# Kernel tuning notes

Hardware: AMD Instinct MI355X
Metric: run time of the kernel (lower is better)

Reference implementation:

```python
import jax, jax.numpy as jnp
import numpy as np

B, N, C, L = 32, 1024, 1024, 16  # batch, pixels (HW), channels, visual tokens


def setup_inputs() -> dict:
    key = jax.random.key(0)
    ks = jax.random.split(key, 18)
    s = lambda fan_in: 1.0 / np.sqrt(fan_in)
    def lin(kw, kb, fin, fout):
        W = jax.random.uniform(kw, (fin, fout), jnp.float32, -s(fin), s(fin))
        b = jax.random.uniform(kb, (fout,), jnp.float32, -s(fin), s(fin))
        return W, b
    tok_W, tok_b = lin(ks[0], ks[1], C, L)          # tokenizer pointwise conv
    key_W, key_b = lin(ks[2], ks[3], C, C // 2)     # transformer key proj
    query_W, query_b = lin(ks[4], ks[5], C, C // 2) # transformer query proj
    f1_W, f1_b = lin(ks[6], ks[7], C, C)            # FFN 1
    f2_W, f2_b = lin(ks[8], ks[9], C, C)            # FFN 2
    q_W, q_b = lin(ks[10], ks[11], C, C)            # projector W_q
    k_W, k_b = lin(ks[12], ks[13], C, C)            # projector W_k
    feature_map = jax.random.normal(ks[14], (B, N, C), jnp.float32)
    T_in = jnp.zeros((B, L, C), jnp.float32)  # unused by FilterBasedTokenizer
    return dict(feature_map=feature_map, T_in=T_in,
                tok_W=tok_W, tok_b=tok_b, key_W=key_W, key_b=key_b,
                query_W=query_W, query_b=query_b, f1_W=f1_W, f1_b=f1_b,
                f2_W=f2_W, f2_b=f2_b, q_W=q_W, q_b=q_b, k_W=k_W, k_b=k_b)


def reference(feature_map, T_in, tok_W, tok_b, key_W, key_b, query_W, query_b,
              f1_W, f1_b, f2_W, f2_b, q_W, q_b, k_W, k_b):
    X = feature_map  # [B, N, C]
    # --- FilterBasedTokenizer: softmax over pixel dim, aggregate pixels -> tokens
    proj = X @ tok_W + tok_b                         # [B, N, L]
    attn = jax.nn.softmax(proj, axis=1)              # softmax over N (dim=1)
    T = jnp.einsum('bnl,bnc->blc', attn, X)          # [B, L, C]
    # --- Transformer block on visual tokens
    k = T @ key_W + key_b                            # [B, L, C/2]
    q = T @ query_W + query_b                        # [B, L, C/2]
    scores = jnp.einsum('bld,bmd->blm', k, q)        # [B, L, L]
    T_dash = T + jax.nn.softmax(scores, axis=2) @ T  # self-attn residual
    T_out = T_dash + (jax.nn.relu(T_dash @ f1_W + f1_b) @ f2_W + f2_b)
    # --- Projector: pixels attend to tokens
    sim = jnp.einsum('bnc,blc->bnl', X @ q_W + q_b, T_out @ k_W + k_b)  # [B, N, L]
    X_out = X + jax.nn.softmax(sim, axis=2) @ T_out  # [B, N, C]
    return (X_out, T_out)
```

## Files before the change

kernel.cpp:

```cpp
#include <hip/hip_runtime.h>
#include <hip/hip_bf16.h>
#include <stdint.h>

#define BB 32
#define NN 1024
#define CC 1024
#define LL 16

typedef __attribute__((ext_vector_type(4))) float f32x4;
typedef __attribute__((ext_vector_type(8))) short short8;
typedef __attribute__((ext_vector_type(4))) unsigned short ushort4v;

__device__ __forceinline__ unsigned short f2bf(float f) {
  union { float f; unsigned u; } v; v.f = f;
  unsigned r = v.u + 0x7FFF + ((v.u >> 16) & 1);
  return (unsigned short)(r >> 16);
}
__device__ __forceinline__ float bf2f(unsigned short h) {
  union { unsigned u; float f; } v; v.u = ((unsigned)h) << 16; return v.f;
}

__global__ __launch_bounds__(256) void wprep(
    const float* __restrict__ keyW, const float* __restrict__ queryW,
    const float* __restrict__ f1W, const float* __restrict__ f2W,
    const float* __restrict__ kW, const float* __restrict__ qW,
    const float* __restrict__ tokW, const float* __restrict__ keyb,
    const float* __restrict__ queryb,
    unsigned short* __restrict__ WkqT, unsigned short* __restrict__ f1WT,
    unsigned short* __restrict__ f2WT, unsigned short* __restrict__ kWT,
    unsigned short* __restrict__ qWbf, unsigned short* __restrict__ tokWT,
    float* __restrict__ biaskq)
{
  int z = blockIdx.z;
  int tx = threadIdx.x, ty = threadIdx.y;
  if (z == 5) {
    int gid = (blockIdx.y * 32 + blockIdx.x) * 256 + ty * 32 + tx;
    if (gid < 16384) {
      int l = gid >> 10, c = gid & 1023;
      tokWT[gid] = f2bf(tokW[c * 16 + l]);
    } else if (gid < 17408) {
      int i = gid - 16384;
      biaskq[i] = (i < 512) ? keyb[i] : queryb[i - 512];
    }
    return;
  }
  if (z == 4) {
#pragma unroll
    for (int i = 0; i < 4; ++i) {
      int row = blockIdx.y * 32 + ty + 8 * i;
      int col = blockIdx.x * 32 + tx;
      qWbf[row * 1024 + col] = f2bf(qW[row * 1024 + col]);
    }
    return;
  }
  __shared__ float tile[32][33];
  int j0 = blockIdx.x * 32, k0 = blockIdx.y * 32;
  const float* src = (z == 1) ? f1W : (z == 2) ? f2W : kW;
#pragma unroll
  for (int i = 0; i < 4; ++i) {
    int k = k0 + ty + 8 * i;
    int j = j0 + tx;
    float v;
    if (z == 0) v = (j < 512) ? keyW[k * 512 + j] : queryW[k * 512 + (j - 512)];
    else        v = src[k * 1024 + j];
    tile[ty + 8 * i][tx] = v;
  }
  __syncthreads();
  unsigned short* dst = (z == 0) ? WkqT : (z == 1) ? f1WT : (z == 2) ? f2WT : kWT;
#pragma unroll
  for (int i = 0; i < 4; ++i) {
    int j = j0 + ty + 8 * i;
    dst[j * 1024 + k0 + tx] = f2bf(tile[tx][ty + 8 * i]);
  }
}

__global__ __launch_bounds__(256) void proj_mfma(
    const float* __restrict__ X, const unsigned short* __restrict__ Wt,
    const float* __restrict__ bias, float* __restrict__ out)
{
  __shared__ __align__(16) char sp[16384];
  int tid = threadIdx.x, wid = tid >> 6, lane = tid & 63;
  int lr = lane & 15, hi = lane >> 4;
  int pix0 = blockIdx.x * 64;
  int b = pix0 >> 10;
  int row = tid >> 2, seg = tid & 3;
  const float* xr = X + (size_t)(pix0 + row) * 1024 + seg * 32;
  const unsigned short* Wb = Wt + (size_t)lr * 1024 + hi * 8;
  int wbyte[4];
#pragma unroll
  for (int u = 0; u < 4; ++u)
    wbyte[u] = row * 256 + (((seg * 64 + u * 16) ^ ((row & 7) << 4)));
  int arow = wid * 16 + lr;
  int rbyte = arow * 256;
  int rx = (arow & 7) << 4;
  f32x4 acc = (f32x4)0.f;
  for (int k0 = 0; k0 < 1024; k0 += 128) {
    f32x4 v[8];
#pragma unroll
    for (int i = 0; i < 8; ++i) v[i] = *(const f32x4*)(xr + k0 + i * 4);
    __syncthreads();
#pragma unroll
    for (int u = 0; u < 4; ++u) {
      short8 pk;
      pk[0] = (short)f2bf(v[2*u][0]);   pk[1] = (short)f2bf(v[2*u][1]);
      pk[2] = (short)f2bf(v[2*u][2]);   pk[3] = (short)f2bf(v[2*u][3]);
      pk[4] = (short)f2bf(v[2*u+1][0]); pk[5] = (short)f2bf(v[2*u+1][1]);
      pk[6] = (short)f2bf(v[2*u+1][2]); pk[7] = (short)f2bf(v[2*u+1][3]);
      *(short8*)(sp + wbyte[u]) = pk;
    }
    __syncthreads();
#pragma unroll
    for (int kk = 0; kk < 4; ++kk) {
      short8 af = *(const short8*)(sp + rbyte + (((kk * 64 + hi * 16) ^ rx)));
      short8 bf = *(const short8*)(Wb + k0 + kk * 32);
      acc = __builtin_amdgcn_mfma_f32_16x16x32_bf16(af, bf, acc, 0, 0, 0);
    }
  }
  int pixb = pix0 + wid * 16 + hi * 4;
  float bv = bias[lr];
#pragma unroll
  for (int rr = 0; rr < 4; ++rr) {
    int pix = pixb + rr;
    out[((size_t)b * 16 + lr) * 1024 + (pix & 1023)] = acc[rr] + bv;
  }
}

__global__ __launch_bounds__(256) void softmax_n(float* __restrict__ projT) {
  float* row = projT + (size_t)blockIdx.x * NN;
  int t = threadIdx.x;
  f32x4 v = ((f32x4*)row)[t];
  float m = fmaxf(fmaxf(v[0], v[1]), fmaxf(v[2], v[3]));
#pragma unroll
  for (int msk = 32; msk >= 1; msk >>= 1) m = fmaxf(m, __shfl_xor(m, msk));
  __shared__ float redm[4], reds[4];
  if ((t & 63) == 0) redm[t >> 6] = m;
  __syncthreads();
  m = fmaxf(fmaxf(redm[0], redm[1]), fmaxf(redm[2], redm[3]));
  f32x4 e;
  e[0] = __expf(v[0] - m); e[1] = __expf(v[1] - m);
  e[2] = __expf(v[2] - m); e[3] = __expf(v[3] - m);
  float s = e[0] + e[1] + e[2] + e[3];
#pragma unroll
  for (int msk = 32; msk >= 1; msk >>= 1) s += __shfl_xor(s, msk);
  if ((t & 63) == 0) reds[t >> 6] = s;
  __syncthreads();
  s = reds[0] + reds[1] + reds[2] + reds[3];
  float inv = 1.f / s;
  e[0] *= inv; e[1] *= inv; e[2] *= inv; e[3] *= inv;
  ((f32x4*)row)[t] = e;
}

__global__ __launch_bounds__(256) void tpart_kernel(
    const float* __restrict__ X, const float* __restrict__ attnT,
    unsigned short* __restrict__ TpartBf)
{
  int b = blockIdx.y, ch = blockIdx.x;
  int n0 = ch * 128;
  __shared__ float att[128][16];
  int tid = threadIdx.x;
#pragma unroll
  for (int i = 0; i < 2; ++i) {
    int fi = tid + 256 * i;
    int l = fi >> 5, n4 = (fi & 31) << 2;
    f32x4 a = *(const f32x4*)&attnT[((size_t)b * 16 + l) * 1024 + n0 + n4];
    att[n4 + 0][l] = a[0]; att[n4 + 1][l] = a[1];
    att[n4 + 2][l] = a[2]; att[n4 + 3][l] = a[3];
  }
  __syncthreads();
  f32x4 acc[16];
#pragma unroll
  for (int l = 0; l < 16; ++l) acc[l] = (f32x4)0.f;
  const float* xp = X + ((size_t)b * 1024 + n0) * 1024 + tid * 4;
#pragma unroll 4
  for (int n = 0; n < 128; ++n) {
    f32x4 xv = *(const f32x4*)(xp + (size_t)n * 1024);
    const f32x4* ar = (const f32x4*)&att[n][0];
    f32x4 a0 = ar[0], a1 = ar[1], a2 = ar[2], a3 = ar[3];
    acc[0]  += a0[0]*xv; acc[1]  += a0[1]*xv; acc[2]  += a0[2]*xv; acc[3]  += a0[3]*xv;
    acc[4]  += a1[0]*xv; acc[5]  += a1[1]*xv; acc[6]  += a1[2]*xv; acc[7]  += a1[3]*xv;
    acc[8]  += a2[0]*xv; acc[9]  += a2[1]*xv; acc[10] += a2[2]*xv; acc[11] += a2[3]*xv;
    acc[12] += a3[0]*xv; acc[13] += a3[1]*xv; acc[14] += a3[2]*xv; acc[15] += a3[3]*xv;
  }
  unsigned short* op = TpartBf + (size_t)(b * 8 + ch) * 16 * 1024 + tid * 4;
#pragma unroll
  for (int l = 0; l < 16; ++l) {
    f32x4 s = acc[l];
    ushort4v h; h[0]=f2bf(s[0]); h[1]=f2bf(s[1]); h[2]=f2bf(s[2]); h[3]=f2bf(s[3]);
    *(ushort4v*)(op + (size_t)l * 1024) = h;
  }
}

__global__ void treduce(const unsigned short* __restrict__ TpartBf,
                        float* __restrict__ T, unsigned short* __restrict__ Tbf) {
  int f = blockIdx.x * 256 + threadIdx.x;
  int b = f >> 12, w = f & 4095;
  f32x4 s = (f32x4)0.f;
#pragma unroll
  for (int ch = 0; ch < 8; ++ch) {
    ushort4v h = ((const ushort4v*)TpartBf)[(size_t)(b * 8 + ch) * 4096 + w];
    s[0] += bf2f(h[0]); s[1] += bf2f(h[1]); s[2] += bf2f(h[2]); s[3] += bf2f(h[3]);
  }
  ((f32x4*)T)[f] = s;
  ushort4v h; h[0]=f2bf(s[0]); h[1]=f2bf(s[1]); h[2]=f2bf(s[2]); h[3]=f2bf(s[3]);
  ((ushort4v*)Tbf)[f] = h;
}

template<int RELU, int HAS_BIAS, int HAS_RES, int STORE_F32, int STORE_BF16>
__global__ __launch_bounds__(256) void gemm32x64(
    const unsigned short* __restrict__ A, const unsigned short* __restrict__ Bm,
    const float* __restrict__ bias, const float* __restrict__ res,
    float* __restrict__ outF, unsigned short* __restrict__ outB)
{
  const int K = 1024;
  __shared__ __align__(16) char sh[12288];
  char* Asp = sh;
  char* Bsp = sh + 4096;
  int tid = threadIdx.x, wid = tid >> 6, lane = tid & 63;
  int lr = lane & 15, hi = lane >> 4;
  int m0 = blockIdx.x * 32, n0 = blockIdx.y * 64;
  int arow = tid >> 3, acol = (tid & 7) * 8;
  int brow = tid >> 2, bcol = (tid & 3) * 16;
  const unsigned short* Ap = A + (size_t)(m0 + arow) * K + acol;
  const unsigned short* Bp = Bm + (size_t)(n0 + brow) * K + bcol;
  int aw  = arow * 128 + (((acol * 2) ^ ((arow & 7) << 4)));
  int bw0 = brow * 128 + (((bcol * 2) ^ ((brow & 7) << 4)));
  int bw1 = brow * 128 + ((((bcol * 2) + 16) ^ ((brow & 7) << 4)));
  short8 aR[2]; short8 bR[2][2];
  aR[0]    = *(const short8*)(Ap);
  bR[0][0] = *(const short8*)(Bp);
  bR[0][1] = *(const short8*)(Bp + 8);
  aR[1]    = *(const short8*)(Ap + 64);
  bR[1][0] = *(const short8*)(Bp + 64);
  bR[1][1] = *(const short8*)(Bp + 72);
  f32x4 acc[2];
  acc[0] = (f32x4)0.f; acc[1] = (f32x4)0.f;
  int wm = (wid >> 1) * 16, wn = (wid & 1) * 32;
  int arb = (wm + lr) * 128, arx = ((wm + lr) & 7) << 4;
  for (int s = 0; s < 16; ++s) {
    __syncthreads();
    *(short8*)(Asp + aw)  = aR[s & 1];
    *(short8*)(Bsp + bw0) = bR[s & 1][0];
    *(short8*)(Bsp + bw1) = bR[s & 1][1];
    __syncthreads();
    if (s + 2 < 16) {
      int k0 = (s + 2) * 64;
      aR[s & 1]    = *(const short8*)(Ap + k0);
      bR[s & 1][0] = *(const short8*)(Bp + k0);
      bR[s & 1][1] = *(const short8*)(Bp + k0 + 8);
    }
#pragma unroll
    for (int kk = 0; kk < 2; ++kk) {
      short8 af = *(const short8*)(Asp + arb + (((kk * 64 + hi * 16) ^ arx)));
#pragma unroll
      for (int sn = 0; sn < 2; ++sn) {
        int br = wn + sn * 16 + lr;
        short8 bf = *(const short8*)(Bsp + br * 128 + (((kk * 64 + hi * 16) ^ ((br & 7) << 4))));
        acc[sn] = __builtin_amdgcn_mfma_f32_16x16x32_bf16(af, bf, acc[sn], 0, 0, 0);
      }
    }
  }
  int row0 = m0 + wm + hi * 4;
#pragma unroll
  for (int sn = 0; sn < 2; ++sn) {
    int col = n0 + wn + sn * 16 + lr;
    float bv_ = HAS_BIAS ? bias[col] : 0.f;
#pragma unroll
    for (int rr = 0; rr < 4; ++rr) {
      float x = acc[sn][rr] + bv_;
      if (RELU) x = fmaxf(x, 0.f);
      size_t idx = (size_t)(row0 + rr) * 1024 + col;
      if (HAS_RES) x += res[idx];
      if (STORE_F32) outF[idx] = x;
      if (STORE_BF16) outB[idx] = f2bf(x);
    }
  }
}

__global__ __launch_bounds__(256) void scores_tdash(
    const float* __restrict__ kq, const float* __restrict__ T,
    float* __restrict__ Tdash, unsigned short* __restrict__ Tdbf)
{
  int cs = blockIdx.x, b = blockIdx.y;
  int c0 = cs * 128;
  __shared__ float Ts[16][128];
  int tid = threadIdx.x, lane = tid & 63;
#pragma unroll
  for (int i = 0; i < 2; ++i) {
    int fi = tid + 256 * i;
    int rrow = fi >> 5, c4 = (fi & 31) * 4;
    *(f32x4*)&Ts[rrow][c4] = *(const f32x4*)&T[((size_t)b * 16 + rrow) * 1024 + c0 + c4];
  }
  __syncthreads();
  int l = tid >> 4, m = tid & 15;
  const float* krow = kq + ((size_t)b * 16 + l) * 1024;
  const float* qrow = kq + ((size_t)b * 16 + m) * 1024 + 512;
  float s = 0.f;
#pragma unroll 8
  for (int d = 0; d < 512; d += 4) {
    f32x4 kv = *(const f32x4*)(krow + d);
    f32x4 qv = *(const f32x4*)(qrow + d);
    s += kv[0]*qv[0] + kv[1]*qv[1] + kv[2]*qv[2] + kv[3]*qv[3];
  }
  float mx = s;
  mx = fmaxf(mx, __shfl_xor(mx, 1)); mx = fmaxf(mx, __shfl_xor(mx, 2));
  mx = fmaxf(mx, __shfl_xor(mx, 4)); mx = fmaxf(mx, __shfl_xor(mx, 8));
  float e = __expf(s - mx);
  float sum = e;
  sum += __shfl_xor(sum, 1); sum += __shfl_xor(sum, 2);
  sum += __shfl_xor(sum, 4); sum += __shfl_xor(sum, 8);
  float pv = e / sum;
  float pl[16];
#pragma unroll
  for (int i = 0; i < 16; ++i) pl[i] = __shfl(pv, (lane & 48) + i);
  float* od = Tdash + ((size_t)b * 16 + l) * 1024 + c0;
  unsigned short* ob = Tdbf + ((size_t)b * 16 + l) * 1024 + c0;
#pragma unroll
  for (int h = 0; h < 2; ++h) {
    int c = m * 8 + h * 4;
    f32x4 o = *(const f32x4*)&Ts[l][c];
#pragma unroll
    for (int mm = 0; mm < 16; ++mm) {
      f32x4 tv = *(const f32x4*)&Ts[mm][c];
      o += pl[mm] * tv;
    }
    *(f32x4*)(od + c) = o;
    ushort4v hh; hh[0]=f2bf(o[0]); hh[1]=f2bf(o[1]); hh[2]=f2bf(o[2]); hh[3]=f2bf(o[3]);
    *(ushort4v*)(ob + c) = hh;
  }
}

__global__ __launch_bounds__(256) void r_kernel(
    const unsigned short* __restrict__ Tkbf, const float* __restrict__ qb,
    float* __restrict__ r)
{
  int row = blockIdx.x * 4 + (threadIdx.x >> 6);
  int lane = threadIdx.x & 63;
  const unsigned short* p = Tkbf + (size_t)row * CC;
  float s = 0.f;
#pragma unroll
  for (int h = 0; h < 2; ++h) {
    int d0 = lane * 8 + h * 512;
    short8 v = *(const short8*)&p[d0];
#pragma unroll
    for (int jj = 0; jj < 8; ++jj)
      s += bf2f((unsigned short)v[jj]) * qb[d0 + jj];
  }
#pragma unroll
  for (int msk = 32; msk >= 1; msk >>= 1) s += __shfl_xor(s, msk);
  if (lane == 0) r[row] = s;
}

__global__ __launch_bounds__(256) void sim_out_kernel(
    const float* __restrict__ X, const unsigned short* __restrict__ Gt,
    const float* __restrict__ rbias, const float* __restrict__ Tout,
    float* __restrict__ Xout)
{
  __shared__ __align__(16) char sp[16384];
  __shared__ float Ps[64][16];
  int tid = threadIdx.x, wid = tid >> 6, lane = tid & 63;
  int lr = lane & 15, hi = lane >> 4;
  int pix0 = blockIdx.x * 64 + blockIdx.y * 1024;
  int b = blockIdx.y;
  int row = tid >> 2, seg = tid & 3;
  const float* xr = X + (size_t)(pix0 + row) * 1024 + seg * 32;
  const unsigned short* Wb = Gt + (size_t)b * 16 * 1024 + (size_t)lr * 1024 + hi * 8;
  int wbyte[4];
#pragma unroll
  for (int u = 0; u < 4; ++u)
    wbyte[u] = row * 256 + (((seg * 64 + u * 16) ^ ((row & 7) << 4)));
  int arow = wid * 16 + lr;
  int rbyte = arow * 256;
  int rx = (arow & 7) << 4;
  f32x4 acc = (f32x4)0.f;
  for (int k0 = 0; k0 < 1024; k0 += 128) {
    f32x4 v[8];
#pragma unroll
    for (int i = 0; i < 8; ++i) v[i] = *(const f32x4*)(xr + k0 + i * 4);
    __syncthreads();
#pragma unroll
    for (int u = 0; u < 4; ++u) {
      short8 pk;
      pk[0] = (short)f2bf(v[2*u][0]);   pk[1] = (short)f2bf(v[2*u][1]);
      pk[2] = (short)f2bf(v[2*u][2]);   pk[3] = (short)f2bf(v[2*u][3]);
      pk[4] = (short)f2bf(v[2*u+1][0]); pk[5] = (short)f2bf(v[2*u+1][1]);
      pk[6] = (short)f2bf(v[2*u+1][2]); pk[7] = (short)f2bf(v[2*u+1][3]);
      *(short8*)(sp + wbyte[u]) = pk;
    }
    __syncthreads();
#pragma unroll
    for (int kk = 0; kk < 4; ++kk) {
      short8 af = *(const short8*)(sp + rbyte + (((kk * 64 + hi * 16) ^ rx)));
      short8 bf = *(const short8*)(Wb + k0 + kk * 32);
      acc = __builtin_amdgcn_mfma_f32_16x16x32_bf16(af, bf, acc, 0, 0, 0);
    }
  }
  float bv = rbias[b * 16 + lr];
  int prow = wid * 16 + hi * 4;
#pragma unroll
  for (int rr = 0; rr < 4; ++rr) {
    float vv = acc[rr] + bv;
    float mx = vv;
    mx = fmaxf(mx, __shfl_xor(mx, 1)); mx = fmaxf(mx, __shfl_xor(mx, 2));
    mx = fmaxf(mx, __shfl_xor(mx, 4)); mx = fmaxf(mx, __shfl_xor(mx, 8));
    float e = __expf(vv - mx);
    float ss = e;
    ss += __shfl_xor(ss, 1); ss += __shfl_xor(ss, 2);
    ss += __shfl_xor(ss, 4); ss += __shfl_xor(ss, 8);
    Ps[prow + rr][lr] = e / ss;
  }
  __syncthreads();
  int c4 = tid * 4;
  f32x4 tsr[16];
#pragma unroll
  for (int l = 0; l < 16; ++l)
    tsr[l] = *(const f32x4*)&Tout[((size_t)b * 16 + l) * 1024 + c4];
  const float* xp = X + (size_t)pix0 * 1024 + c4;
  float* op = Xout + (size_t)pix0 * 1024 + c4;
#pragma unroll 2
  for (int n = 0; n < 64; ++n) {
    f32x4 xv = *(const f32x4*)(xp + (size_t)n * 1024);
    const f32x4* pr = (const f32x4*)&Ps[n][0];
    f32x4 p0 = pr[0], p1 = pr[1], p2 = pr[2], p3 = pr[3];
    f32x4 o = xv;
    o += p0[0]*tsr[0];  o += p0[1]*tsr[1];  o += p0[2]*tsr[2];  o += p0[3]*tsr[3];
    o += p1[0]*tsr[4];  o += p1[1]*tsr[5];  o += p1[2]*tsr[6];  o += p1[3]*tsr[7];
    o += p2[0]*tsr[8];  o += p2[1]*tsr[9];  o += p2[2]*tsr[10]; o += p2[3]*tsr[11];
    o += p3[0]*tsr[12]; o += p3[1]*tsr[13]; o += p3[2]*tsr[14]; o += p3[3]*tsr[15];
    *(f32x4*)(op + (size_t)n * 1024) = o;
  }
}

extern "C" void kernel_launch(void* const* d_in, const int* in_sizes, int n_in,
                              void* d_out, int out_size, void* d_ws, size_t ws_size,
                              hipStream_t stream)
{
  const float* X      = (const float*)d_in[0];
  const float* tokW   = (const float*)d_in[2];
  const float* tokB   = (const float*)d_in[3];
  const float* keyW   = (const float*)d_in[4];
  const float* keyB   = (const float*)d_in[5];
  const float* queryW = (const float*)d_in[6];
  const float* queryB = (const float*)d_in[7];
  const float* f1W    = (const float*)d_in[8];
  const float* f1B    = (const float*)d_in[9];
  const float* f2W    = (const float*)d_in[10];
  const float* f2B    = (const float*)d_in[11];
  const float* qW     = (const float*)d_in[12];
  const float* qB     = (const float*)d_in[13];
  const float* kW     = (const float*)d_in[14];
  const float* kB     = (const float*)d_in[15];

  float* Xout = (float*)d_out;
  float* Tout = (float*)d_out + (size_t)BB * NN * CC;

  char* ws = (char*)d_ws;
  size_t off = 0;
  auto alloc_f = [&](size_t n) { float* pp = (float*)(ws + off); off += n * 4; return pp; };
  float* attn   = alloc_f(524288);
  float* Tbuf   = alloc_f(524288);
  float* kqbuf  = alloc_f(524288);
  float* Tdash  = alloc_f(524288);
  float* rbuf   = alloc_f(1024);
  float* biaskq = alloc_f(1024);
  auto alloc_h = [&](size_t n) { unsigned short* pp = (unsigned short*)(ws + off); off += n * 2; return pp; };
  unsigned short* TpartBf = alloc_h(4194304);
  unsigned short* Tbf    = alloc_h(524288);
  unsigned short* Tdbf   = alloc_h(524288);
  unsigned short* Hbf    = alloc_h(524288);
  unsigned short* Toutbf = alloc_h(524288);
  unsigned short* Tkbf   = alloc_h(524288);
  unsigned short* Gtbf   = alloc_h(524288);
  unsigned short* WkqT   = alloc_h(1048576);
  unsigned short* f1WT   = alloc_h(1048576);
  unsigned short* f2WT   = alloc_h(1048576);
  unsigned short* kWT    = alloc_h(1048576);
  unsigned short* qWbf   = alloc_h(1048576);
  unsigned short* tokWT  = alloc_h(16384);
  (void)ws_size; (void)in_sizes; (void)n_in; (void)out_size;

  wprep<<<dim3(32, 32, 6), dim3(32, 8), 0, stream>>>(keyW, queryW, f1W, f2W, kW, qW,
                                                     tokW, keyB, queryB,
                                                     WkqT, f1WT, f2WT, kWT, qWbf, tokWT, biaskq);
  proj_mfma<<<dim3(512), 256, 0, stream>>>(X, tokWT, tokB, attn);
  softmax_n<<<512, 256, 0, stream>>>(attn);
  tpart_kernel<<<dim3(8, 32), 256, 0, stream>>>(X, attn, TpartBf);
  treduce<<<512, 256, 0, stream>>>(TpartBf, Tbuf, Tbf);
  gemm32x64<0,1,0,1,0><<<dim3(16, 16), 256, 0, stream>>>(Tbf, WkqT, biaskq, nullptr, kqbuf, nullptr);
  scores_tdash<<<dim3(8, 32), 256, 0, stream>>>(kqbuf, Tbuf, Tdash, Tdbf);
  gemm32x64<1,1,0,0,1><<<dim3(16, 16), 256, 0, stream>>>(Tdbf, f1WT, f1B, nullptr, nullptr, Hbf);
  gemm32x64<0,1,1,1,1><<<dim3(16, 16), 256, 0, stream>>>(Hbf, f2WT, f2B, Tdash, Tout, Toutbf);
  gemm32x64<0,1,0,0,1><<<dim3(16, 16), 256, 0, stream>>>(Toutbf, kWT, kB, nullptr, nullptr, Tkbf);
  r_kernel<<<128, 256, 0, stream>>>(Tkbf, qB, rbuf);
  gemm32x64<0,0,0,0,1><<<dim3(16, 16), 256, 0, stream>>>(Tkbf, qWbf, nullptr, nullptr, nullptr, Gtbf);
  sim_out_kernel<<<dim3(16, 32), 256, 0, stream>>>(X, Gtbf, rbuf, Tout, Xout);
}
```

Measured before the change: 210.6 us.

## Fuse tokenizer with online softmax and run chain as one cooperative kernel

The projection, softmax over pixels and token aggregation are merged into one kernel that emits per-chunk unnormalized partial tokens plus local max and sum statistics, which are combined flash-style in a merge stage. The remaining small GEMMs, scores, r and sim_out stages run inside a single cooperative kernel of 256 blocks separated by grid syncs, replacing about ten separate launches. This removes the attention buffer round trip and most per-launch gaps. In exchange, sim_out now uses only 256 blocks with 128 pixels each, which lowers parallelism for the largest memory-bound stage, and the code depends on cooperative launch support.

```diff
diff --git a/kernel.cpp b/kernel.cpp
--- a/kernel.cpp
+++ b/kernel.cpp
@@ -1,6 +1,9 @@
 #include <hip/hip_runtime.h>
 #include <hip/hip_bf16.h>
+#include <hip/hip_cooperative_groups.h>
 #include <stdint.h>
+
+namespace cg = cooperative_groups;
 
 #define BB 32
 #define NN 1024
@@ -74,33 +77,38 @@
   }
 }
 
-__global__ __launch_bounds__(256) void proj_mfma(
-    const float* __restrict__ X, const unsigned short* __restrict__ Wt,
-    const float* __restrict__ bias, float* __restrict__ out)
+__global__ __launch_bounds__(256) void tok_fused(
+    const float* __restrict__ X, const unsigned short* __restrict__ tokWT,
+    const float* __restrict__ tokB, unsigned short* __restrict__ Tp,
+    float* __restrict__ Mloc, float* __restrict__ Sloc)
 {
-  __shared__ __align__(16) char sp[16384];
+  __shared__ __align__(16) char sp[32768];
+  __shared__ float E[128][16];
+  __shared__ float redm[4][16];
+  __shared__ float reds[4][16];
   int tid = threadIdx.x, wid = tid >> 6, lane = tid & 63;
   int lr = lane & 15, hi = lane >> 4;
-  int pix0 = blockIdx.x * 64;
-  int b = pix0 >> 10;
-  int row = tid >> 2, seg = tid & 3;
-  const float* xr = X + (size_t)(pix0 + row) * 1024 + seg * 32;
-  const unsigned short* Wb = Wt + (size_t)lr * 1024 + hi * 8;
-  int wbyte[4];
-#pragma unroll
-  for (int u = 0; u < 4; ++u)
-    wbyte[u] = row * 256 + (((seg * 64 + u * 16) ^ ((row & 7) << 4)));
-  int arow = wid * 16 + lr;
-  int rbyte = arow * 256;
-  int rx = (arow & 7) << 4;
-  f32x4 acc = (f32x4)0.f;
+  int b = blockIdx.y, ch = blockIdx.x;
+  int pix0 = b * 1024 + ch * 128;
+  int row = tid >> 1, half = tid & 1;
+  const float* xr = X + (size_t)(pix0 + row) * 1024 + half * 64;
+  const unsigned short* Wb = tokWT + lr * 1024 + hi * 8;
+  int wbyte[8];
+#pragma unroll
+  for (int u = 0; u < 8; ++u)
+    wbyte[u] = row * 256 + (((half * 128 + u * 16) ^ ((row & 7) << 4)));
+  int arow0 = wid * 32;
+  int ar0 = arow0 + lr, ar1 = arow0 + 16 + lr;
+  int arb0 = ar0 * 256, arx0 = (ar0 & 7) << 4;
+  int arb1 = ar1 * 256, arx1 = (ar1 & 7) << 4;
+  f32x4 acc0 = (f32x4)0.f, acc1 = (f32x4)0.f;
   for (int k0 = 0; k0 < 1024; k0 += 128) {
-    f32x4 v[8];
-#pragma unroll
-    for (int i = 0; i < 8; ++i) v[i] = *(const f32x4*)(xr + k0 + i * 4);
+    f32x4 v[16];
+#pragma unroll
+    for (int i = 0; i < 16; ++i) v[i] = *(const f32x4*)(xr + k0 + i * 4);
     __syncthreads();
 #pragma unroll
-    for (int u = 0; u < 4; ++u) {
+    for (int u = 0; u < 8; ++u) {
       short8 pk;
       pk[0] = (short)f2bf(v[2*u][0]);   pk[1] = (short)f2bf(v[2*u][1]);
       pk[2] = (short)f2bf(v[2*u][2]);   pk[3] = (short)f2bf(v[2*u][3]);
@@ -111,113 +119,126 @@
     __syncthreads();
 #pragma unroll
     for (int kk = 0; kk < 4; ++kk) {
-      short8 af = *(const short8*)(sp + rbyte + (((kk * 64 + hi * 16) ^ rx)));
-      short8 bf = *(const short8*)(Wb + k0 + kk * 32);
-      acc = __builtin_amdgcn_mfma_f32_16x16x32_bf16(af, bf, acc, 0, 0, 0);
-    }
-  }
-  int pixb = pix0 + wid * 16 + hi * 4;
-  float bv = bias[lr];
+      short8 bfv = *(const short8*)(Wb + k0 + kk * 32);
+      short8 a0 = *(const short8*)(sp + arb0 + (((kk * 64 + hi * 16) ^ arx0)));
+      short8 a1 = *(const short8*)(sp + arb1 + (((kk * 64 + hi * 16) ^ arx1)));
+      acc0 = __builtin_amdgcn_mfma_f32_16x16x32_bf16(a0, bfv, acc0, 0, 0, 0);
+      acc1 = __builtin_amdgcn_mfma_f32_16x16x32_bf16(a1, bfv, acc1, 0, 0, 0);
+    }
+  }
+  float tb = tokB[lr];
+  float sv[8];
+#pragma unroll
+  for (int rr = 0; rr < 4; ++rr) { sv[rr] = acc0[rr] + tb; sv[4 + rr] = acc1[rr] + tb; }
+  float pm = sv[0];
+#pragma unroll
+  for (int i = 1; i < 8; ++i) pm = fmaxf(pm, sv[i]);
+  pm = fmaxf(pm, __shfl_xor(pm, 16));
+  pm = fmaxf(pm, __shfl_xor(pm, 32));
+  if (hi == 0) redm[wid][lr] = pm;
+  __syncthreads();
+  float m = fmaxf(fmaxf(redm[0][lr], redm[1][lr]), fmaxf(redm[2][lr], redm[3][lr]));
+  float ev[8]; float ps = 0.f;
+#pragma unroll
+  for (int i = 0; i < 8; ++i) { ev[i] = __expf(sv[i] - m); ps += ev[i]; }
+  ps += __shfl_xor(ps, 16); ps += __shfl_xor(ps, 32);
+  if (hi == 0) reds[wid][lr] = ps;
 #pragma unroll
   for (int rr = 0; rr < 4; ++rr) {
-    int pix = pixb + rr;
-    out[((size_t)b * 16 + lr) * 1024 + (pix & 1023)] = acc[rr] + bv;
-  }
-}
-
-__global__ __launch_bounds__(256) void softmax_n(float* __restrict__ projT) {
-  float* row = projT + (size_t)blockIdx.x * NN;
-  int t = threadIdx.x;
-  f32x4 v = ((f32x4*)row)[t];
-  float m = fmaxf(fmaxf(v[0], v[1]), fmaxf(v[2], v[3]));
-#pragma unroll
-  for (int msk = 32; msk >= 1; msk >>= 1) m = fmaxf(m, __shfl_xor(m, msk));
-  __shared__ float redm[4], reds[4];
-  if ((t & 63) == 0) redm[t >> 6] = m;
+    E[arow0 + hi * 4 + rr][lr] = ev[rr];
+    E[arow0 + 16 + hi * 4 + rr][lr] = ev[4 + rr];
+  }
   __syncthreads();
-  m = fmaxf(fmaxf(redm[0], redm[1]), fmaxf(redm[2], redm[3]));
-  f32x4 e;
-  e[0] = __expf(v[0] - m); e[1] = __expf(v[1] - m);
-  e[2] = __expf(v[2] - m); e[3] = __expf(v[3] - m);
-  float s = e[0] + e[1] + e[2] + e[3];
-#pragma unroll
-  for (int msk = 32; msk >= 1; msk >>= 1) s += __shfl_xor(s, msk);
-  if ((t & 63) == 0) reds[t >> 6] = s;
-  __syncthreads();
-  s = reds[0] + reds[1] + reds[2] + reds[3];
-  float inv = 1.f / s;
-  e[0] *= inv; e[1] *= inv; e[2] *= inv; e[3] *= inv;
-  ((f32x4*)row)[t] = e;
-}
-
-__global__ __launch_bounds__(256) void tpart_kernel(
-    const float* __restrict__ X, const float* __restrict__ attnT,
-    unsigned short* __restrict__ TpartBf)
-{
-  int b = blockIdx.y, ch = blockIdx.x;
-  int n0 = ch * 128;
-  __shared__ float att[128][16];
-  int tid = threadIdx.x;
-#pragma unroll
-  for (int i = 0; i < 2; ++i) {
-    int fi = tid + 256 * i;
-    int l = fi >> 5, n4 = (fi & 31) << 2;
-    f32x4 a = *(const f32x4*)&attnT[((size_t)b * 16 + l) * 1024 + n0 + n4];
-    att[n4 + 0][l] = a[0]; att[n4 + 1][l] = a[1];
-    att[n4 + 2][l] = a[2]; att[n4 + 3][l] = a[3];
-  }
-  __syncthreads();
-  f32x4 acc[16];
-#pragma unroll
-  for (int l = 0; l < 16; ++l) acc[l] = (f32x4)0.f;
-  const float* xp = X + ((size_t)b * 1024 + n0) * 1024 + tid * 4;
+  if (tid < 16) {
+    float sl = reds[0][tid] + reds[1][tid] + reds[2][tid] + reds[3][tid];
+    Mloc[(b * 8 + ch) * 16 + tid] = m;
+    Sloc[(b * 8 + ch) * 16 + tid] = sl;
+  }
+  f32x4 a16[16];
+#pragma unroll
+  for (int l = 0; l < 16; ++l) a16[l] = (f32x4)0.f;
+  const float* xp = X + (size_t)pix0 * 1024 + tid * 4;
 #pragma unroll 4
   for (int n = 0; n < 128; ++n) {
     f32x4 xv = *(const f32x4*)(xp + (size_t)n * 1024);
-    const f32x4* ar = (const f32x4*)&att[n][0];
+    const f32x4* ar = (const f32x4*)&E[n][0];
     f32x4 a0 = ar[0], a1 = ar[1], a2 = ar[2], a3 = ar[3];
-    acc[0]  += a0[0]*xv; acc[1]  += a0[1]*xv; acc[2]  += a0[2]*xv; acc[3]  += a0[3]*xv;
-    acc[4]  += a1[0]*xv; acc[5]  += a1[1]*xv; acc[6]  += a1[2]*xv; acc[7]  += a1[3]*xv;
-    acc[8]  += a2[0]*xv; acc[9]  += a2[1]*xv; acc[10] += a2[2]*xv; acc[11] += a2[3]*xv;
-    acc[12] += a3[0]*xv; acc[13] += a3[1]*xv; acc[14] += a3[2]*xv; acc[15] += a3[3]*xv;
-  }
-  unsigned short* op = TpartBf + (size_t)(b * 8 + ch) * 16 * 1024 + tid * 4;
+    a16[0]  += a0[0]*xv; a16[1]  += a0[1]*xv; a16[2]  += a0[2]*xv; a16[3]  += a0[3]*xv;
+    a16[4]  += a1[0]*xv; a16[5]  += a1[1]*xv; a16[6]  += a1[2]*xv; a16[7]  += a1[3]*xv;
+    a16[8]  += a2[0]*xv; a16[9]  += a2[1]*xv; a16[10] += a2[2]*xv; a16[11] += a2[3]*xv;
+    a16[12] += a3[0]*xv; a16[13] += a3[1]*xv; a16[14] += a3[2]*xv; a16[15] += a3[3]*xv;
+  }
+  unsigned short* op = Tp + ((size_t)(b * 8 + ch) * 16) * 1024 + tid * 4;
 #pragma unroll
   for (int l = 0; l < 16; ++l) {
-    f32x4 s = acc[l];
+    f32x4 s = a16[l];
     ushort4v h; h[0]=f2bf(s[0]); h[1]=f2bf(s[1]); h[2]=f2bf(s[2]); h[3]=f2bf(s[3]);
     *(ushort4v*)(op + (size_t)l * 1024) = h;
   }
 }
 
-__global__ void treduce(const unsigned short* __restrict__ TpartBf,
-                        float* __restrict__ T, unsigned short* __restrict__ Tbf) {
-  int f = blockIdx.x * 256 + threadIdx.x;
-  int b = f >> 12, w = f & 4095;
-  f32x4 s = (f32x4)0.f;
+struct ChainArgs {
+  const unsigned short* Tp; const float* Mloc; const float* Sloc;
+  float* Tbuf; unsigned short* Tbf;
+  const unsigned short* WkqT; const float* biaskq; float* kqbuf;
+  float* Tdash; unsigned short* Tdbf;
+  const unsigned short* f1WT; const float* f1B; unsigned short* Hbf;
+  const unsigned short* f2WT; const float* f2B; float* Tout; unsigned short* Toutbf;
+  const unsigned short* kWT; const float* kB; unsigned short* Tkbf;
+  const unsigned short* qWbf; const float* qB; float* rbuf;
+  unsigned short* Gtbf;
+  const float* X; float* Xout;
+};
+
+__device__ __forceinline__ void tmerge_stage(int bid, const ChainArgs& a) {
+  int tid = threadIdx.x;
+  int g = bid * 2 + (tid >> 7);
+  int b = g >> 4, l = g & 15;
+  int j = tid & 127;
+  float M = -1e30f;
+#pragma unroll
+  for (int ch = 0; ch < 8; ++ch) M = fmaxf(M, a.Mloc[(b * 8 + ch) * 16 + l]);
+  float w[8]; float denom = 0.f;
 #pragma unroll
   for (int ch = 0; ch < 8; ++ch) {
-    ushort4v h = ((const ushort4v*)TpartBf)[(size_t)(b * 8 + ch) * 4096 + w];
-    s[0] += bf2f(h[0]); s[1] += bf2f(h[1]); s[2] += bf2f(h[2]); s[3] += bf2f(h[3]);
-  }
-  ((f32x4*)T)[f] = s;
-  ushort4v h; h[0]=f2bf(s[0]); h[1]=f2bf(s[1]); h[2]=f2bf(s[2]); h[3]=f2bf(s[3]);
-  ((ushort4v*)Tbf)[f] = h;
+    w[ch] = __expf(a.Mloc[(b * 8 + ch) * 16 + l] - M);
+    denom += w[ch] * a.Sloc[(b * 8 + ch) * 16 + l];
+  }
+  float inv = 1.f / denom;
+  float o[8];
+#pragma unroll
+  for (int t = 0; t < 8; ++t) o[t] = 0.f;
+#pragma unroll
+  for (int ch = 0; ch < 8; ++ch) {
+    const unsigned short* p = a.Tp + ((size_t)((b * 8 + ch) * 16 + l)) * 1024 + j * 8;
+    short8 v = *(const short8*)p;
+    float wc = w[ch];
+#pragma unroll
+    for (int t = 0; t < 8; ++t) o[t] += wc * bf2f((unsigned short)v[t]);
+  }
+  f32x4 o0, o1; short8 hb;
+#pragma unroll
+  for (int t = 0; t < 4; ++t) {
+    float x0 = o[t] * inv, x1 = o[4 + t] * inv;
+    o0[t] = x0; o1[t] = x1;
+    hb[t] = (short)f2bf(x0); hb[4 + t] = (short)f2bf(x1);
+  }
+  *(f32x4*)(a.Tbuf + (size_t)g * 1024 + j * 8) = o0;
+  *(f32x4*)(a.Tbuf + (size_t)g * 1024 + j * 8 + 4) = o1;
+  *(short8*)(a.Tbf + (size_t)g * 1024 + j * 8) = hb;
 }
 
 template<int RELU, int HAS_BIAS, int HAS_RES, int STORE_F32, int STORE_BF16>
-__global__ __launch_bounds__(256) void gemm32x64(
-    const unsigned short* __restrict__ A, const unsigned short* __restrict__ Bm,
-    const float* __restrict__ bias, const float* __restrict__ res,
-    float* __restrict__ outF, unsigned short* __restrict__ outB)
+__device__ __forceinline__ void gemm_stage(int bid, char* smem,
+    const unsigned short* A, const unsigned short* Bm,
+    const float* bias, const float* res, float* outF, unsigned short* outB)
 {
   const int K = 1024;
-  __shared__ __align__(16) char sh[12288];
-  char* Asp = sh;
-  char* Bsp = sh + 4096;
+  char* Asp = smem;
+  char* Bsp = smem + 4096;
   int tid = threadIdx.x, wid = tid >> 6, lane = tid & 63;
   int lr = lane & 15, hi = lane >> 4;
-  int m0 = blockIdx.x * 32, n0 = blockIdx.y * 64;
+  int m0 = (bid & 15) * 32, n0 = (bid >> 4) * 64;
   int arow = tid >> 3, acol = (tid & 7) * 8;
   int brow = tid >> 2, bcol = (tid & 3) * 16;
   const unsigned short* Ap = A + (size_t)(m0 + arow) * K + acol;
@@ -276,24 +297,21 @@
   }
 }
 
-__global__ __launch_bounds__(256) void scores_tdash(
-    const float* __restrict__ kq, const float* __restrict__ T,
-    float* __restrict__ Tdash, unsigned short* __restrict__ Tdbf)
-{
-  int cs = blockIdx.x, b = blockIdx.y;
+__device__ __forceinline__ void scores_stage(int bid, char* smem, const ChainArgs& a) {
+  float (*Ts)[128] = (float(*)[128])smem;
+  int cs = bid & 7, b = bid >> 3;
   int c0 = cs * 128;
-  __shared__ float Ts[16][128];
   int tid = threadIdx.x, lane = tid & 63;
 #pragma unroll
   for (int i = 0; i < 2; ++i) {
     int fi = tid + 256 * i;
     int rrow = fi >> 5, c4 = (fi & 31) * 4;
-    *(f32x4*)&Ts[rrow][c4] = *(const f32x4*)&T[((size_t)b * 16 + rrow) * 1024 + c0 + c4];
+    *(f32x4*)&Ts[rrow][c4] = *(const f32x4*)&a.Tbuf[((size_t)b * 16 + rrow) * 1024 + c0 + c4];
   }
   __syncthreads();
   int l = tid >> 4, m = tid & 15;
-  const float* krow = kq + ((size_t)b * 16 + l) * 1024;
-  const float* qrow = kq + ((size_t)b * 16 + m) * 1024 + 512;
+  const float* krow = a.kqbuf + ((size_t)b * 16 + l) * 1024;
+  const float* qrow = a.kqbuf + ((size_t)b * 16 + m) * 1024 + 512;
   float s = 0.f;
 #pragma unroll 8
   for (int d = 0; d < 512; d += 4) {
@@ -312,8 +330,8 @@
   float pl[16];
 #pragma unroll
   for (int i = 0; i < 16; ++i) pl[i] = __shfl(pv, (lane & 48) + i);
-  float* od = Tdash + ((size_t)b * 16 + l) * 1024 + c0;
-  unsigned short* ob = Tdbf + ((size_t)b * 16 + l) * 1024 + c0;
+  float* od = a.Tdash + ((size_t)b * 16 + l) * 1024 + c0;
+  unsigned short* ob = a.Tdbf + ((size_t)b * 16 + l) * 1024 + c0;
 #pragma unroll
   for (int h = 0; h < 2; ++h) {
     int c = m * 8 + h * 4;
@@ -329,56 +347,52 @@
   }
 }
 
-__global__ __launch_bounds__(256) void r_kernel(
-    const unsigned short* __restrict__ Tkbf, const float* __restrict__ qb,
-    float* __restrict__ r)
-{
-  int row = blockIdx.x * 4 + (threadIdx.x >> 6);
-  int lane = threadIdx.x & 63;
-  const unsigned short* p = Tkbf + (size_t)row * CC;
-  float s = 0.f;
-#pragma unroll
-  for (int h = 0; h < 2; ++h) {
-    int d0 = lane * 8 + h * 512;
-    short8 v = *(const short8*)&p[d0];
-#pragma unroll
-    for (int jj = 0; jj < 8; ++jj)
-      s += bf2f((unsigned short)v[jj]) * qb[d0 + jj];
-  }
-#pragma unroll
-  for (int msk = 32; msk >= 1; msk >>= 1) s += __shfl_xor(s, msk);
-  if (lane == 0) r[row] = s;
-}
-
-__global__ __launch_bounds__(256) void sim_out_kernel(
-    const float* __restrict__ X, const unsigned short* __restrict__ Gt,
-    const float* __restrict__ rbias, const float* __restrict__ Tout,
-    float* __restrict__ Xout)
-{
-  __shared__ __align__(16) char sp[16384];
-  __shared__ float Ps[64][16];
+__device__ __forceinline__ void r_stage(int bid, const ChainArgs& a) {
+  int tid = threadIdx.x, wid = tid >> 6, lane = tid & 63;
+#pragma unroll
+  for (int rw = 0; rw < 8; ++rw) {
+    int m = bid * 32 + wid * 8 + rw;
+    const unsigned short* p = a.Tkbf + (size_t)m * 1024 + lane * 16;
+    short8 v0 = *(const short8*)p;
+    short8 v1 = *(const short8*)(p + 8);
+    float s = 0.f;
+#pragma unroll
+    for (int j = 0; j < 8; ++j) {
+      s += bf2f((unsigned short)v0[j]) * a.qB[lane * 16 + j];
+      s += bf2f((unsigned short)v1[j]) * a.qB[lane * 16 + 8 + j];
+    }
+#pragma unroll
+    for (int msk = 32; msk >= 1; msk >>= 1) s += __shfl_xor(s, msk);
+    if (lane == 0) a.rbuf[m] = s;
+  }
+}
+
+__device__ __forceinline__ void simout_stage(int bid, char* smem, const ChainArgs& a) {
+  char* sp = smem;
+  float (*Ps)[16] = (float(*)[16])(smem + 32768);
   int tid = threadIdx.x, wid = tid >> 6, lane = tid & 63;
   int lr = lane & 15, hi = lane >> 4;
-  int pix0 = blockIdx.x * 64 + blockIdx.y * 1024;
-  int b = blockIdx.y;
-  int row = tid >> 2, seg = tid & 3;
-  const float* xr = X + (size_t)(pix0 + row) * 1024 + seg * 32;
-  const unsigned short* Wb = Gt + (size_t)b * 16 * 1024 + (size_t)lr * 1024 + hi * 8;
-  int wbyte[4];
-#pragma unroll
-  for (int u = 0; u < 4; ++u)
-    wbyte[u] = row * 256 + (((seg * 64 + u * 16) ^ ((row & 7) << 4)));
-  int arow = wid * 16 + lr;
-  int rbyte = arow * 256;
-  int rx = (arow & 7) << 4;
-  f32x4 acc = (f32x4)0.f;
+  int b = bid >> 3, ch = bid & 7;
+  int pix0 = b * 1024 + ch * 128;
+  int row = tid >> 1, half = tid & 1;
+  const float* xr = a.X + (size_t)(pix0 + row) * 1024 + half * 64;
+  const unsigned short* Wb = a.Gtbf + (size_t)b * 16 * 1024 + (size_t)lr * 1024 + hi * 8;
+  int wbyte[8];
+#pragma unroll
+  for (int u = 0; u < 8; ++u)
+    wbyte[u] = row * 256 + (((half * 128 + u * 16) ^ ((row & 7) << 4)));
+  int arow0 = wid * 32;
+  int ar0 = arow0 + lr, ar1 = arow0 + 16 + lr;
+  int arb0 = ar0 * 256, arx0 = (ar0 & 7) << 4;
+  int arb1 = ar1 * 256, arx1 = (ar1 & 7) << 4;
+  f32x4 acc0 = (f32x4)0.f, acc1 = (f32x4)0.f;
   for (int k0 = 0; k0 < 1024; k0 += 128) {
-    f32x4 v[8];
-#pragma unroll
-    for (int i = 0; i < 8; ++i) v[i] = *(const f32x4*)(xr + k0 + i * 4);
+    f32x4 v[16];
+#pragma unroll
+    for (int i = 0; i < 16; ++i) v[i] = *(const f32x4*)(xr + k0 + i * 4);
     __syncthreads();
 #pragma unroll
-    for (int u = 0; u < 4; ++u) {
+    for (int u = 0; u < 8; ++u) {
       short8 pk;
       pk[0] = (short)f2bf(v[2*u][0]);   pk[1] = (short)f2bf(v[2*u][1]);
       pk[2] = (short)f2bf(v[2*u][2]);   pk[3] = (short)f2bf(v[2*u][3]);
@@ -389,16 +403,17 @@
     __syncthreads();
 #pragma unroll
     for (int kk = 0; kk < 4; ++kk) {
-      short8 af = *(const short8*)(sp + rbyte + (((kk * 64 + hi * 16) ^ rx)));
-      short8 bf = *(const short8*)(Wb + k0 + kk * 32);
-      acc = __builtin_amdgcn_mfma_f32_16x16x32_bf16(af, bf, acc, 0, 0, 0);
-    }
-  }
-  float bv = rbias[b * 16 + lr];
-  int prow = wid * 16 + hi * 4;
-#pragma unroll
-  for (int rr = 0; rr < 4; ++rr) {
-    float vv = acc[rr] + bv;
+      short8 bfv = *(const short8*)(Wb + k0 + kk * 32);
+      short8 a0 = *(const short8*)(sp + arb0 + (((kk * 64 + hi * 16) ^ arx0)));
+      short8 a1 = *(const short8*)(sp + arb1 + (((kk * 64 + hi * 16) ^ arx1)));
+      acc0 = __builtin_amdgcn_mfma_f32_16x16x32_bf16(a0, bfv, acc0, 0, 0, 0);
+      acc1 = __builtin_amdgcn_mfma_f32_16x16x32_bf16(a1, bfv, acc1, 0, 0, 0);
+    }
+  }
+  float bv = a.rbuf[b * 16 + lr];
+#pragma unroll
+  for (int q = 0; q < 8; ++q) {
+    float vv = (q < 4 ? acc0[q] : acc1[q - 4]) + bv;
     float mx = vv;
     mx = fmaxf(mx, __shfl_xor(mx, 1)); mx = fmaxf(mx, __shfl_xor(mx, 2));
     mx = fmaxf(mx, __shfl_xor(mx, 4)); mx = fmaxf(mx, __shfl_xor(mx, 8));
@@ -406,18 +421,18 @@
     float ss = e;
     ss += __shfl_xor(ss, 1); ss += __shfl_xor(ss, 2);
     ss += __shfl_xor(ss, 4); ss += __shfl_xor(ss, 8);
-    Ps[prow + rr][lr] = e / ss;
+    Ps[arow0 + (q < 4 ? 0 : 16) + hi * 4 + (q & 3)][lr] = e / ss;
   }
   __syncthreads();
   int c4 = tid * 4;
   f32x4 tsr[16];
 #pragma unroll
   for (int l = 0; l < 16; ++l)
-    tsr[l] = *(const f32x4*)&Tout[((size_t)b * 16 + l) * 1024 + c4];
-  const float* xp = X + (size_t)pix0 * 1024 + c4;
-  float* op = Xout + (size_t)pix0 * 1024 + c4;
+    tsr[l] = *(const f32x4*)&a.Tout[((size_t)b * 16 + l) * 1024 + c4];
+  const float* xp = a.X + (size_t)pix0 * 1024 + c4;
+  float* op = a.Xout + (size_t)pix0 * 1024 + c4;
 #pragma unroll 2
-  for (int n = 0; n < 64; ++n) {
+  for (int n = 0; n < 128; ++n) {
     f32x4 xv = *(const f32x4*)(xp + (size_t)n * 1024);
     const f32x4* pr = (const f32x4*)&Ps[n][0];
     f32x4 p0 = pr[0], p1 = pr[1], p2 = pr[2], p3 = pr[3];
@@ -426,8 +441,30 @@
     o += p1[0]*tsr[4];  o += p1[1]*tsr[5];  o += p1[2]*tsr[6];  o += p1[3]*tsr[7];
     o += p2[0]*tsr[8];  o += p2[1]*tsr[9];  o += p2[2]*tsr[10]; o += p2[3]*tsr[11];
     o += p3[0]*tsr[12]; o += p3[1]*tsr[13]; o += p3[2]*tsr[14]; o += p3[3]*tsr[15];
-    *(f32x4*)(op + (size_t)n * 1024) = o;
-  }
+    __builtin_nontemporal_store(o, (f32x4*)(op + (size_t)n * 1024));
+  }
+}
+
+__global__ __launch_bounds__(256) void chain_kernel(ChainArgs a) {
+  cg::grid_group gg = cg::this_grid();
+  __shared__ __align__(16) char smem[40960];
+  int bid = blockIdx.x;
+  tmerge_stage(bid, a);
+  gg.sync();
+  gemm_stage<0,1,0,1,0>(bid, smem, a.Tbf, a.WkqT, a.biaskq, nullptr, a.kqbuf, nullptr);
+  gg.sync();
+  scores_stage(bid, smem, a);
+  gg.sync();
+  gemm_stage<1,1,0,0,1>(bid, smem, a.Tdbf, a.f1WT, a.f1B, nullptr, nullptr, a.Hbf);
+  gg.sync();
+  gemm_stage<0,1,1,1,1>(bid, smem, a.Hbf, a.f2WT, a.f2B, a.Tdash, a.Tout, a.Toutbf);
+  gg.sync();
+  gemm_stage<0,1,0,0,1>(bid, smem, a.Toutbf, a.kWT, a.kB, nullptr, nullptr, a.Tkbf);
+  gg.sync();
+  gemm_stage<0,0,0,0,1>(bid, smem, a.Tkbf, a.qWbf, nullptr, nullptr, nullptr, a.Gtbf);
+  if (bid < 16) r_stage(bid, a);
+  gg.sync();
+  simout_stage(bid, smem, a);
 }
 
 extern "C" void kernel_launch(void* const* d_in, const int* in_sizes, int n_in,
@@ -456,14 +493,15 @@
   char* ws = (char*)d_ws;
   size_t off = 0;
   auto alloc_f = [&](size_t n) { float* pp = (float*)(ws + off); off += n * 4; return pp; };
-  float* attn   = alloc_f(524288);
   float* Tbuf   = alloc_f(524288);
   float* kqbuf  = alloc_f(524288);
   float* Tdash  = alloc_f(524288);
   float* rbuf   = alloc_f(1024);
   float* biaskq = alloc_f(1024);
+  float* Mloc   = alloc_f(4096);
+  float* Sloc   = alloc_f(4096);
   auto alloc_h = [&](size_t n) { unsigned short* pp = (unsigned short*)(ws + off); off += n * 2; return pp; };
-  unsigned short* TpartBf = alloc_h(4194304);
+  unsigned short* Tp     = alloc_h(4194304);
   unsigned short* Tbf    = alloc_h(524288);
   unsigned short* Tdbf   = alloc_h(524288);
   unsigned short* Hbf    = alloc_h(524288);
@@ -481,16 +519,19 @@
   wprep<<<dim3(32, 32, 6), dim3(32, 8), 0, stream>>>(keyW, queryW, f1W, f2W, kW, qW,
                                                      tokW, keyB, queryB,
                                                      WkqT, f1WT, f2WT, kWT, qWbf, tokWT, biaskq);
-  proj_mfma<<<dim3(512), 256, 0, stream>>>(X, tokWT, tokB, attn);
-  softmax_n<<<512, 256, 0, stream>>>(attn);
-  tpart_kernel<<<dim3(8, 32), 256, 0, stream>>>(X, attn, TpartBf);
-  treduce<<<512, 256, 0, stream>>>(TpartBf, Tbuf, Tbf);
-  gemm32x64<0,1,0,1,0><<<dim3(16, 16), 256, 0, stream>>>(Tbf, WkqT, biaskq, nullptr, kqbuf, nullptr);
-  scores_tdash<<<dim3(8, 32), 256, 0, stream>>>(kqbuf, Tbuf, Tdash, Tdbf);
-  gemm32x64<1,1,0,0,1><<<dim3(16, 16), 256, 0, stream>>>(Tdbf, f1WT, f1B, nullptr, nullptr, Hbf);
-  gemm32x64<0,1,1,1,1><<<dim3(16, 16), 256, 0, stream>>>(Hbf, f2WT, f2B, Tdash, Tout, Toutbf);
-  gemm32x64<0,1,0,0,1><<<dim3(16, 16), 256, 0, stream>>>(Toutbf, kWT, kB, nullptr, nullptr, Tkbf);
-  r_kernel<<<128, 256, 0, stream>>>(Tkbf, qB, rbuf);
-  gemm32x64<0,0,0,0,1><<<dim3(16, 16), 256, 0, stream>>>(Tkbf, qWbf, nullptr, nullptr, nullptr, Gtbf);
-  sim_out_kernel<<<dim3(16, 32), 256, 0, stream>>>(X, Gtbf, rbuf, Tout, Xout);
-}
+  tok_fused<<<dim3(8, 32), 256, 0, stream>>>(X, tokWT, tokB, Tp, Mloc, Sloc);
+
+  ChainArgs ca;
+  ca.Tp = Tp; ca.Mloc = Mloc; ca.Sloc = Sloc;
+  ca.Tbuf = Tbuf; ca.Tbf = Tbf;
+  ca.WkqT = WkqT; ca.biaskq = biaskq; ca.kqbuf = kqbuf;
+  ca.Tdash = Tdash; ca.Tdbf = Tdbf;
+  ca.f1WT = f1WT; ca.f1B = f1B; ca.Hbf = Hbf;
+  ca.f2WT = f2WT; ca.f2B = f2B; ca.Tout = Tout; ca.Toutbf = Toutbf;
+  ca.kWT = kWT; ca.kB = kB; ca.Tkbf = Tkbf;
+  ca.qWbf = qWbf; ca.qB = qB; ca.rbuf = rbuf;
+  ca.Gtbf = Gtbf;
+  ca.X = X; ca.Xout = Xout;
+  void* kp[] = { &ca };
+  hipLaunchCooperativeKernel((void*)chain_kernel, dim3(256), dim3(256), kp, 0, stream);
+}
```

Measured after the change: 422.6 us. 101% more time.
